# Kernel tuning notes

Measured on AMD Instinct MI355X. Metric: run time of the kernel, lower is better.

The kernel has to match this reference:

```python
import jax, jax.numpy as jnp
import numpy as np
from jax import lax

P = 8       # patch_size
TEMP = 30.0 # softmax temperature from RelationUnit.temp


def _conv3x3(x, w, b, groups):
    # x: [B, C, H, W], w: [O, C//groups, 3, 3]
    y = lax.conv_general_dilated(x, w, (1, 1), 'SAME', feature_group_count=groups)
    return y + b[None, :, None, None]


def _unfold(x):
    # nn.Unfold(kernel=P, stride=P): [B,C,H,W] -> [B, C*P*P, n], channel-major then (ki,kj)
    B, C, H, W = x.shape
    x = x.reshape(B, C, H // P, P, W // P, P)
    x = x.transpose(0, 1, 3, 5, 2, 4)          # [B,C,P,P,H/P,W/P]
    return x.reshape(B, C * P * P, (H // P) * (W // P))


def _fold(x, H, W):
    # inverse of _unfold (non-overlapping patches)
    B, CPP, n = x.shape
    C = CPP // (P * P)
    x = x.reshape(B, C, P, P, H // P, W // P)
    x = x.transpose(0, 1, 4, 2, 5, 3)          # [B,C,H/P,P,W/P,P]
    return x.reshape(B, C, H, W)


def _head(query, key, value, wq, bq, wk, bk, wv, bv):
    # one RelationUnit (heads=1 internally)
    b, tq, c, h, w = query.shape
    t = key.shape[1]
    n = (h // P) * (w // P)
    d = P * P * c

    q = _conv3x3(query.reshape(-1, c, h, w), wq, bq, groups=c)   # depthwise
    k = _conv3x3(key.reshape(-1, c, h, w), wk, bk, groups=c)     # depthwise
    v = _conv3x3(value.reshape(-1, c, h, w), wv, bv, groups=1)   # dense

    # [b*t, d, n] -> [b, d, t*n]  (matches view/permute chain in torch code)
    uq = _unfold(q).reshape(b, tq, d, n).transpose(0, 2, 1, 3).reshape(b, d, tq * n)
    uk = _unfold(k).reshape(b, t, d, n).transpose(0, 2, 1, 3).reshape(b, d, t * n)
    uv = _unfold(v).reshape(b, t, d, n).transpose(0, 2, 1, 3).reshape(b, d, t * n)

    attn = jnp.einsum('bdq,bdk->bqk', uq, uk) * (d ** -0.5)
    attn = jax.nn.softmax(attn * TEMP, axis=-1)
    out = jnp.einsum('bqk,bdk->bqd', attn, uv)                   # [b, tq*n, d]

    out = out.reshape(b, tq, n, d).transpose(0, 1, 3, 2).reshape(b * tq, d, n)
    feat = _fold(out, h, w)                                      # [b*tq, c, h, w]
    return feat.reshape(query.shape)


def reference(query, key, value, Wq, bq, Wk, bk, Wv, bv):
    heads = jax.vmap(_head, in_axes=(None, None, None, 0, 0, 0, 0, 0, 0))(
        query, key, value, Wq, bq, Wk, bk, Wv, bv)               # [Nh, b, tq, c, h, w]
    Nh = heads.shape[0]
    return jnp.concatenate([heads[i] for i in range(Nh)], axis=-1)


def setup_inputs() -> dict:
    key = jax.random.key(0)
    ks = jax.random.split(key, 6)
    b, tq, t, c, h, w, Nh = 1, 2, 2, 32, 224, 336, 4
    f32 = jnp.float32
    rn = lambda k, s, sc=1.0: jax.random.normal(k, s, f32) * sc
    return {
        'query': rn(ks[0], (b, tq, c, h, w)),
        'key':   rn(ks[1], (b, t, c, h, w)),
        'value': rn(ks[2], (b, t, c, h, w)),
        'Wq': rn(ks[3], (Nh, c, 1, 3, 3), 0.1), 'bq': jnp.zeros((Nh, c), f32),
        'Wk': rn(ks[4], (Nh, c, 1, 3, 3), 0.1), 'bk': jnp.zeros((Nh, c), f32),
        'Wv': rn(ks[5], (Nh, c, c, 3, 3), 0.05), 'bv': jnp.zeros((Nh, c), f32),
    }
```

## Files before the change

### kernel.cpp

```cpp
#include <hip/hip_runtime.h>
#include <hip/hip_bf16.h>

#define T_FR 2
#define C_CH 32
#define H_IMG 224
#define W_IMG 336
#define NH 4
#define NPATCH 1176
#define NQ 2352
#define NPAD 2432
#define DD 2048
#define WOUT (W_IMG*NH)
#define SM_SCALE 0.6629126073623885f
#define PIX_F (H_IMG*W_IMG)
#define PIX_T (T_FR*PIX_F)

typedef __attribute__((ext_vector_type(4))) float f32x4;
typedef __attribute__((ext_vector_type(8))) short short8;
typedef unsigned short ushort_t;
typedef __attribute__((ext_vector_type(4))) unsigned short u16x4;
typedef __attribute__((ext_vector_type(8))) unsigned short u16x8;

__device__ inline ushort_t f2bf(float x){
  union { float f; unsigned int u; } v; v.f = x;
  unsigned int r = v.u + 0x7fffu + ((v.u >> 16) & 1u);
  return (ushort_t)(r >> 16);
}

__device__ inline void gload16(const void* g, void* l){
  __builtin_amdgcn_global_load_lds(
      (const __attribute__((address_space(1))) void*)g,
      (__attribute__((address_space(3))) void*)l,
      16, 0, 0);
}

__global__ __launch_bounds__(256) void zero_pads(
    ushort_t* __restrict__ Qu, ushort_t* __restrict__ Ku,
    ushort_t* __restrict__ Vu, int nh)
{
  const int per = 80*DD;
  int tot = 3*nh*per;
  for (int id = blockIdx.x*256 + threadIdx.x; id < tot; id += gridDim.x*256){
    int buf = id / (nh*per);
    int rem = id - buf*(nh*per);
    int h = rem / per;
    int e = rem - h*per;
    ushort_t* B = (buf==0) ? Qu : (buf==1) ? Ku : Vu;
    B[((size_t)h*NPAD + NQ)*DD + e] = 0;
  }
}

__global__ __launch_bounds__(256) void transpose_cl(
    const float* __restrict__ in, ushort_t* __restrict__ inCL)
{
  int id = blockIdx.x*256 + threadIdx.x;
  int t = id / PIX_F;
  int p = id - t*PIX_F;
  const float* src = in + (size_t)t*C_CH*PIX_F + p;
  #pragma unroll
  for (int oct=0; oct<4; oct++){
    u16x8 u;
    #pragma unroll
    for (int e=0; e<8; e++)
      u[e] = f2bf(src[(size_t)(oct*8+e)*PIX_F]);
    *(u16x8*)&inCL[(size_t)id*C_CH + oct*8] = u;
  }
}

__global__ __launch_bounds__(256) void prep_wb(
    const float* __restrict__ Wv, ushort_t* __restrict__ Wb)
{
  int idx = blockIdx.x*256 + threadIdx.x;
  if (idx >= 9*128*32) return;
  int tap = idx >> 12;
  int og  = (idx >> 5) & 127;
  int cc  = idx & 31;
  Wb[idx] = f2bf(Wv[(size_t)og*288 + cc*9 + tap]);
}

__global__ __launch_bounds__(256) void dwconv_unfold(
    const float* __restrict__ in, const float* __restrict__ Wd,
    const float* __restrict__ bd, ushort_t* __restrict__ outU,
    int head0, int nh)
{
  int id = blockIdx.x*256 + threadIdx.x;
  int cc = id & 31;
  int rest = id >> 5;
  int xseg = rest % 42;
  rest /= 42;
  int y = rest % H_IMG;
  int t = rest / H_IMG;

  const float* src = in + ((size_t)(t*C_CH + cc)*H_IMG)*W_IMG;
  int x0 = xseg*8;

  float r0[10], r1[10], r2[10];
  #pragma unroll
  for (int j=0;j<10;j++){
    int xx = x0 + j - 1;
    bool xok = (xx>=0) && (xx<W_IMG);
    r0[j] = (xok && y>0)         ? src[(size_t)(y-1)*W_IMG+xx] : 0.f;
    r1[j] = (xok)                ? src[(size_t)y*W_IMG+xx]     : 0.f;
    r2[j] = (xok && y<H_IMG-1)   ? src[(size_t)(y+1)*W_IMG+xx] : 0.f;
  }
  int qrow = t*NPATCH + (y>>3)*42 + xseg;
  int dcol = (y&7)*256 + cc*8;

  for (int h = 0; h < nh; ++h){
    const float* w = Wd + ((size_t)(head0+h)*C_CH + cc)*9;
    float w0=w[0],w1=w[1],w2=w[2],w3=w[3],w4=w[4],w5=w[5],w6=w[6],w7=w[7],w8=w[8];
    float bias = bd[(size_t)(head0+h)*C_CH + cc];
    u16x8 res;
    #pragma unroll
    for (int j=0;j<8;j++){
      float a = bias;
      a += r0[j]*w0 + r0[j+1]*w1 + r0[j+2]*w2;
      a += r1[j]*w3 + r1[j+1]*w4 + r1[j+2]*w5;
      a += r2[j]*w6 + r2[j+1]*w7 + r2[j+2]*w8;
      res[j] = f2bf(a);
    }
    *(u16x8*)&outU[((size_t)h*NPAD + qrow)*DD + dcol] = res;
  }
}

#define VA_HALO 0
#define VA_BS   37120
#define V_LDS   73984

__global__ __launch_bounds__(256) void vconv_mfma(
    const ushort_t* __restrict__ inCL, const ushort_t* __restrict__ Wb,
    const float* __restrict__ bvv, ushort_t* __restrict__ Vu, int head0)
{
  __shared__ __align__(16) char lds[V_LDS];
  int xt = blockIdx.x;
  int pr_g = blockIdx.y;
  int z  = blockIdx.z;
  int t  = pr_g / 28, pr = pr_g - t*28;
  int x0 = xt*56, y0 = pr*8;
  int tid = threadIdx.x, lane = tid & 63, wid = tid >> 6;

  for (int i = tid; i < 580; i += 256){
    int ly = i/58, lx = i - (i/58)*58;
    int gy = y0 - 1 + ly, gx = x0 - 1 + lx;
    u16x8 v0={},v1={},v2={},v3={};
    if (gy>=0 && gy<H_IMG && gx>=0 && gx<W_IMG){
      const u16x8* s = (const u16x8*)&inCL[((size_t)t*PIX_F + gy*W_IMG + gx)*C_CH];
      v0=s[0]; v1=s[1]; v2=s[2]; v3=s[3];
    }
    *(u16x8*)&lds[VA_HALO + 0*9280 + i*16] = v0;
    *(u16x8*)&lds[VA_HALO + 1*9280 + i*16] = v1;
    *(u16x8*)&lds[VA_HALO + 2*9280 + i*16] = v2;
    *(u16x8*)&lds[VA_HALO + 3*9280 + i*16] = v3;
  }
  for (int i = tid; i < 576; i += 256){
    int tap = i/64, ol = i - (i/64)*64;
    const u16x8* s = (const u16x8*)&Wb[((size_t)tap*128 + head0*32 + z*64 + ol)*C_CH];
    #pragma unroll
    for (int oct=0; oct<4; oct++)
      *(u16x8*)&lds[VA_BS + tap*4096 + ol*64 + ((oct^(ol&3))<<4)] = s[oct];
  }
  __syncthreads();

  int aoff[7];
  #pragma unroll
  for (int m=0;m<7;m++){
    int pm = wid*112 + m*16 + (lane&15);
    int yl = pm/56, xl = pm - yl*56;
    aoff[m] = VA_HALO + (lane>>4)*9280 + (yl*58 + xl)*16;
  }

  f32x4 acc[7][4] = {};
  #pragma unroll
  for (int tap=0; tap<9; tap++){
    const int dy = tap/3, dx = tap - (tap/3)*3;
    short8 bfr[4];
    #pragma unroll
    for (int n=0;n<4;n++){
      int ol = n*16 + (lane&15);
      bfr[n] = *(const short8*)&lds[VA_BS + tap*4096 + ol*64 + ((((lane>>4))^(ol&3))<<4)];
    }
    #pragma unroll
    for (int m=0;m<7;m++){
      short8 af = *(const short8*)&lds[aoff[m] + (dy*58+dx)*16];
      #pragma unroll
      for (int n=0;n<4;n++)
        acc[m][n] = __builtin_amdgcn_mfma_f32_16x16x32_bf16(af, bfr[n], acc[m][n], 0,0,0);
    }
  }
  __syncthreads();

  float bias[4];
  #pragma unroll
  for (int n=0;n<4;n++){
    int ol = n*16 + (lane&15);
    bias[n] = bvv[(size_t)(head0 + z*2 + (ol>>5))*C_CH + (ol&31)];
  }
  #pragma unroll
  for (int m=0;m<7;m++){
    #pragma unroll
    for (int j=0;j<4;j++){
      int p = wid*112 + m*16 + (lane>>4)*4 + j;
      int yl = p/56, xl = p - (p/56)*56;
      int kl = xl >> 3;
      int off = yl*8 + (xl&7);
      #pragma unroll
      for (int n=0;n<4;n++){
        int ol = n*16 + (lane&15);
        int addr = ((ol>>5)*7 + kl)*4096 + (off*32 + (ol&31))*2;
        *(ushort_t*)&lds[addr] = f2bf(acc[m][n][j] + bias[n]);
      }
    }
  }
  __syncthreads();
  int key0 = t*NPATCH + pr*42 + xt*7;
  #pragma unroll
  for (int i=0;i<14;i++){
    int c = i*256 + tid;
    int hib = c / 1792;
    int rem = c - hib*1792;
    int kl = rem >> 8, dch = rem & 255;
    u16x8 v = *(const u16x8*)&lds[c*16];
    *(u16x8*)&Vu[((size_t)(z*2+hib)*NPAD + key0 + kl)*DD + dch*8] = v;
  }
}

__global__ __launch_bounds__(256) void vtranspose(
    const ushort_t* __restrict__ Vu, ushort_t* __restrict__ Vt)
{
  __shared__ ushort_t tile[64*68];
  int d0 = blockIdx.x*64;
  int k0 = blockIdx.y*64;
  const ushort_t* src = Vu + (size_t)blockIdx.z*NPAD*DD;
  ushort_t* dst = Vt + (size_t)blockIdx.z*DD*NPAD;
  int t = threadIdx.x;
  #pragma unroll
  for (int i=0;i<2;i++){
    int key = (t>>3) + i*32;
    int dd  = (t&7)*8;
    u16x8 v = *(const u16x8*)&src[(size_t)(k0+key)*DD + d0+dd];
    #pragma unroll
    for (int e=0;e<8;e++) tile[(dd+e)*68 + key] = v[e];
  }
  __syncthreads();
  #pragma unroll
  for (int i=0;i<2;i++){
    int dd  = (t>>3) + i*32;
    int key = (t&7)*8;
    u16x4 a = *(const u16x4*)&tile[dd*68 + key];
    u16x4 b = *(const u16x4*)&tile[dd*68 + key + 4];
    u16x8 v;
    v[0]=a[0]; v[1]=a[1]; v[2]=a[2]; v[3]=a[3];
    v[4]=b[0]; v[5]=b[1]; v[6]=b[2]; v[7]=b[3];
    *(u16x8*)&dst[(size_t)(d0+dd)*NPAD + k0+key] = v;
  }
}

#define ABASE(b,kc) ((b)*32768 + (kc)*16384)
#define BBASE(b,kc) (65536 + (b)*32768 + (kc)*16384)

#define STG(dstb, Mat, t0, Rm1, ktc) { \
  int i0_ = tid;       int r0_ = i0_>>2; int c0_ = ((i0_&3) ^ ((r0_>>1)&3)); \
  gload16(Mat + (size_t)min(t0 + r0_, Rm1)*(size_t)K + (ktc) + c0_*8, \
          lds + (dstb) + (tid & ~63)*16); \
  int i1_ = 512 + tid; int r1_ = i1_>>2; int c1_ = ((i1_&3) ^ ((r1_>>1)&3)); \
  gload16(Mat + (size_t)min(t0 + r1_, Rm1)*(size_t)K + (ktc) + c1_*8, \
          lds + (dstb) + (512 + (tid & ~63))*16); }

#define RD_A(dst, b, kc, mh) { _Pragma("unroll") \
  for (int m=0;m<4;m++) \
    dst[m] = *(const short8*)(lds + ABASE(b,kc) + (wr*128 + (mh)*64 + m*16 + l15)*64 + rkB); }

#define RD_B(dst, b, kc) { _Pragma("unroll") \
  for (int n=0;n<4;n++) \
    dst[n] = *(const short8*)(lds + BBASE(b,kc) + (wc*64 + n*16 + l15)*64 + rkB); }

#define MFMA32() { __builtin_amdgcn_s_setprio(1); \
  _Pragma("unroll") for (int m=0;m<4;m++){ \
    _Pragma("unroll") for (int n=0;n<4;n++) \
      acc[m][n] = __builtin_amdgcn_mfma_f32_16x16x32_bf16(af[m], bf[n], acc[m][n], 0,0,0); } \
  _Pragma("unroll") for (int m=0;m<4;m++){ \
    _Pragma("unroll") for (int n=0;n<4;n++) \
      acc[4+m][n] = __builtin_amdgcn_mfma_f32_16x16x32_bf16(ag[m], bf[n], acc[4+m][n], 0,0,0); } \
  __builtin_amdgcn_s_setprio(0); }

#define LEADBAR() { __builtin_amdgcn_sched_barrier(0); \
  __builtin_amdgcn_s_barrier(); __builtin_amdgcn_sched_barrier(0); }

#define TRAILBAR() { __builtin_amdgcn_sched_barrier(0); \
  __builtin_amdgcn_s_barrier(); __builtin_amdgcn_sched_barrier(0); }

#define GATEBAR(cond) { __builtin_amdgcn_sched_barrier(0); \
  if (cond) { asm volatile("s_waitcnt vmcnt(4)" ::: "memory"); } \
  else      { asm volatile("s_waitcnt vmcnt(0)" ::: "memory"); } \
  __builtin_amdgcn_s_barrier(); __builtin_amdgcn_sched_barrier(0); }

template<int MODE>
__global__ __launch_bounds__(512) void gemm8p(
    const ushort_t* __restrict__ A, const ushort_t* __restrict__ B,
    float* __restrict__ C, float* __restrict__ Out,
    int K, int Am1, int Bm1, size_t aStr, size_t bStr, int head0)
{
  __shared__ __align__(16) char lds[131072];
  int tid = threadIdx.x, lane = tid & 63, wid = tid >> 6;

  int gx = gridDim.x, gy = gridDim.y;
  int nwg = gx*gy*gridDim.z;
  int id  = (blockIdx.z*gy + blockIdx.y)*gx + blockIdx.x;
  int swz = (id & 7)*(nwg >> 3) + (id >> 3);
  int bx = swz % gx; int tmp = swz / gx;
  int by = tmp % gy; int bz = tmp / gy;

  const ushort_t* Ab = A + (size_t)bz*aStr;
  const ushort_t* Bb = B + (size_t)bz*bStr;
  int row0 = by*256, col0 = bx*256;
  int wr = wid >> 2, wc = wid & 3;
  int l15 = lane & 15;
  int rkB = (((lane>>4) ^ ((l15>>1)&3)) * 16);

  f32x4 acc[8][4] = {};
  int NT = K >> 6;
  int NI = NT >> 1;

  STG(ABASE(0,0), Ab, row0, Am1, 0)
  STG(BBASE(0,0), Bb, col0, Bm1, 0)
  STG(ABASE(0,1), Ab, row0, Am1, 32)
  STG(BBASE(0,1), Bb, col0, Bm1, 32)
  STG(ABASE(1,0), Ab, row0, Am1, 64)
  STG(BBASE(1,0), Bb, col0, Bm1, 64)
  __builtin_amdgcn_sched_barrier(0);
  asm volatile("s_waitcnt vmcnt(4)" ::: "memory");
  __builtin_amdgcn_s_barrier();
  __builtin_amdgcn_sched_barrier(0);

  #pragma unroll 1
  for (int it = 0; it < NI; ++it){
    int T1k = (2*it+1) << 6;
    int T2k = (2*it+2) << 6;
    int T3k = (2*it+3) << 6;
    bool s2 = (2*it+2 < NT), s3 = (2*it+3 < NT);
    short8 af[4], ag[4], bf[4];

    RD_A(af, 0,0,0) RD_A(ag, 0,0,1) RD_B(bf, 0,0)
    STG(ABASE(1,1), Ab, row0, Am1, T1k+32)
    STG(BBASE(1,1), Bb, col0, Bm1, T1k+32)
    LEADBAR() MFMA32() TRAILBAR()
    RD_A(af, 0,1,0) RD_A(ag, 0,1,1) RD_B(bf, 0,1)
    if (s2){ STG(ABASE(0,0), Ab, row0, Am1, T2k)
             STG(BBASE(0,0), Bb, col0, Bm1, T2k) }
    LEADBAR() MFMA32()
    GATEBAR(s2)
    RD_A(af, 1,0,0) RD_A(ag, 1,0,1) RD_B(bf, 1,0)
    if (s2){ STG(ABASE(0,1), Ab, row0, Am1, T2k+32)
             STG(BBASE(0,1), Bb, col0, Bm1, T2k+32) }
    LEADBAR() MFMA32() TRAILBAR()
    RD_A(af, 1,1,0) RD_A(ag, 1,1,1) RD_B(bf, 1,1)
    if (s3){ STG(ABASE(1,0), Ab, row0, Am1, T3k)
             STG(BBASE(1,0), Bb, col0, Bm1, T3k) }
    LEADBAR() MFMA32()
    GATEBAR(s3)
  }
  __builtin_amdgcn_sched_barrier(0);
  asm volatile("s_waitcnt vmcnt(0) lgkmcnt(0)" ::: "memory");
  __builtin_amdgcn_sched_barrier(0);

  int rb0 = row0 + wr*128 + (lane>>4)*4;
  int cb0 = col0 + wc*64 + l15;
  if (MODE == 0){
    float* Cb = C + (size_t)bz*NPAD*(size_t)NPAD;
    #pragma unroll
    for (int M=0;M<8;M++)
      #pragma unroll
      for (int n=0;n<4;n++){
        int col = cb0 + n*16;
        if (col < NPAD)
          #pragma unroll
          for (int j=0;j<4;j++){
            int row = rb0 + M*16 + j;
            if (row < NPAD)
              Cb[(size_t)row*NPAD + col] = acc[M][n][j];
          }
      }
  } else {
    int head = head0 + bz;
    #pragma unroll
    for (int M=0;M<8;M++){
      #pragma unroll
      for (int j=0;j<4;j++){
        int q = rb0 + M*16 + j;
        if (q < NQ){
          int t = q / NPATCH;
          int p = q - t*NPATCH;
          int hi = p / 42, wi = p - hi*42;
          #pragma unroll
          for (int n=0;n<4;n++){
            int dd = cb0 + n*16;
            int cch = dd & 31;
            int off = dd >> 5;
            int pi = off >> 3, pj = off & 7;
            int yy = hi*8 + pi, xx = wi*8 + pj;
            Out[(((size_t)t*C_CH + cch)*H_IMG + yy)*WOUT + (size_t)head*W_IMG + xx]
              = acc[M][n][j];
          }
        }
      }
    }
  }
}

__global__ __launch_bounds__(256) void softmax_rows(
    const float* __restrict__ S, ushort_t* __restrict__ Pm)
{
  const float* row = S + ((size_t)blockIdx.y*NPAD + blockIdx.x)*NPAD;
  ushort_t* prow = Pm + ((size_t)blockIdx.y*NPAD + blockIdx.x)*NPAD;
  int tid = threadIdx.x;
  __shared__ float red[4];
  const f32x4* row4 = (const f32x4*)row;

  bool h2 = (512 + tid) < 588;
  f32x4 v0 = row4[tid];
  f32x4 v1 = row4[256 + tid];
  f32x4 v2 = {-3.0e38f, -3.0e38f, -3.0e38f, -3.0e38f};
  if (h2) v2 = row4[512 + tid];

  float mx = -3.0e38f;
  #pragma unroll
  for (int e=0;e<4;e++) mx = fmaxf(mx, fmaxf(v0[e], fmaxf(v1[e], v2[e])));
  #pragma unroll
  for (int o=32;o;o>>=1) mx = fmaxf(mx, __shfl_xor(mx, o));
  if ((tid&63)==0) red[tid>>6] = mx;
  __syncthreads();
  mx = fmaxf(fmaxf(red[0],red[1]), fmaxf(red[2],red[3]));
  __syncthreads();

  f32x4 e0, e1, e2 = {0.f,0.f,0.f,0.f};
  float s = 0.f;
  #pragma unroll
  for (int e=0;e<4;e++){ e0[e] = __expf((v0[e]-mx)*SM_SCALE); s += e0[e]; }
  #pragma unroll
  for (int e=0;e<4;e++){ e1[e] = __expf((v1[e]-mx)*SM_SCALE); s += e1[e]; }
  if (h2){
    #pragma unroll
    for (int e=0;e<4;e++){ e2[e] = __expf((v2[e]-mx)*SM_SCALE); s += e2[e]; }
  }
  #pragma unroll
  for (int o=32;o;o>>=1) s += __shfl_xor(s, o);
  if ((tid&63)==0) red[tid>>6] = s;
  __syncthreads();
  s = (red[0]+red[1]) + (red[2]+red[3]);
  float inv = 1.0f / s;

  u16x4 o0, o1;
  #pragma unroll
  for (int e=0;e<4;e++) o0[e] = f2bf(e0[e]*inv);
  #pragma unroll
  for (int e=0;e<4;e++) o1[e] = f2bf(e1[e]*inv);
  *(u16x4*)&prow[tid*4]        = o0;
  *(u16x4*)&prow[1024 + tid*4] = o1;
  if (h2){
    u16x4 o2;
    #pragma unroll
    for (int e=0;e<4;e++) o2[e] = f2bf(e2[e]*inv);
    *(u16x4*)&prow[2048 + tid*4] = o2;
  } else if (512 + tid < 608){
    u16x4 z = {0,0,0,0};
    *(u16x4*)&prow[2048 + tid*4] = z;
  }
}

extern "C" void kernel_launch(void* const* d_in, const int* in_sizes, int n_in,
                              void* d_out, int out_size, void* d_ws, size_t ws_size,
                              hipStream_t stream)
{
  const float* query = (const float*)d_in[0];
  const float* key_  = (const float*)d_in[1];
  const float* value = (const float*)d_in[2];
  const float* Wq = (const float*)d_in[3];
  const float* bq = (const float*)d_in[4];
  const float* Wk = (const float*)d_in[5];
  const float* bk = (const float*)d_in[6];
  const float* Wv = (const float*)d_in[7];
  const float* bv = (const float*)d_in[8];
  float* out = (float*)d_out;

  const size_t szU = (size_t)NPAD*DD;
  const size_t szS = (size_t)NPAD*NPAD;
  const size_t perHeadB = 3*szU*sizeof(ushort_t) + szS*sizeof(float) + szS*sizeof(ushort_t);

  int nh = (ws_size >= 4*perHeadB) ? 4 : 2;

  for (int h0 = 0; h0 < NH; h0 += nh){
    char* p = (char*)d_ws;
    ushort_t* Qu = (ushort_t*)p; p += nh*szU*sizeof(ushort_t);
    ushort_t* Ku = (ushort_t*)p; p += nh*szU*sizeof(ushort_t);
    ushort_t* Vu = (ushort_t*)p; p += nh*szU*sizeof(ushort_t);
    float*    S  = (float*)p;    p += nh*szS*sizeof(float);
    ushort_t* Pm = (ushort_t*)p;
    ushort_t* inCL = (ushort_t*)S;
    ushort_t* Wb   = inCL + (size_t)PIX_T*C_CH;
    ushort_t* Vt   = Qu;

    zero_pads<<<dim3(960), dim3(256), 0, stream>>>(Qu, Ku, Vu, nh);
    transpose_cl<<<dim3(588), dim3(256), 0, stream>>>(value, inCL);
    prep_wb<<<dim3(144), dim3(256), 0, stream>>>(Wv, Wb);
    dwconv_unfold<<<dim3(2352), dim3(256), 0, stream>>>(query, Wq, bq, Qu, h0, nh);
    dwconv_unfold<<<dim3(2352), dim3(256), 0, stream>>>(key_,  Wk, bk, Ku, h0, nh);
    vconv_mfma<<<dim3(6, 56, nh/2), dim3(256), 0, stream>>>(inCL, Wb, bv, Vu, h0);
    gemm8p<0><<<dim3(10, 10, nh), dim3(512), 0, stream>>>(
        Qu, Ku, S, nullptr, DD, NPAD-1, NPAD-1, szU, szU, h0);
    vtranspose<<<dim3(32, 38, nh), dim3(256), 0, stream>>>(Vu, Vt);
    softmax_rows<<<dim3(NPAD, nh), dim3(256), 0, stream>>>(S, Pm);
    gemm8p<1><<<dim3(8, 10, nh), dim3(512), 0, stream>>>(
        Pm, Vt, nullptr, out, NPAD, NPAD-1, DD-1, szS, szU, h0);
  }
}
```

Measured before the change: 496.2 us.

## Replace deep LDS pipeline with simple double-buffered 32-wide K loop in GEMM

Rewrites the main GEMM loop to stage one 32-wide K slice per step into a two-slot LDS buffer. This replaces the previous four-stage 64-wide schedule with partial vmcnt waits and halves LDS use from 128 KB to 64 KB, which may allow more resident workgroups per CU. In exchange each step now waits for all outstanding loads (vmcnt(0)) and has more barriers per unit of MFMA work, so less global-load latency is hidden.

```diff
diff --git a/kernel.cpp b/kernel.cpp
--- a/kernel.cpp
+++ b/kernel.cpp
@@ -255,8 +255,8 @@
   }
 }
 
-#define ABASE(b,kc) ((b)*32768 + (kc)*16384)
-#define BBASE(b,kc) (65536 + (b)*32768 + (kc)*16384)
+#define ABASE2(b) ((b)*16384)
+#define BBASE2(b) (32768 + (b)*16384)
 
 #define STG(dstb, Mat, t0, Rm1, ktc) { \
   int i0_ = tid;       int r0_ = i0_>>2; int c0_ = ((i0_&3) ^ ((r0_>>1)&3)); \
@@ -266,32 +266,25 @@
   gload16(Mat + (size_t)min(t0 + r1_, Rm1)*(size_t)K + (ktc) + c1_*8, \
           lds + (dstb) + (512 + (tid & ~63))*16); }
 
-#define RD_A(dst, b, kc, mh) { _Pragma("unroll") \
+#define RD_A(dst, b, mh) { _Pragma("unroll") \
   for (int m=0;m<4;m++) \
-    dst[m] = *(const short8*)(lds + ABASE(b,kc) + (wr*128 + (mh)*64 + m*16 + l15)*64 + rkB); }
-
-#define RD_B(dst, b, kc) { _Pragma("unroll") \
+    dst[m] = *(const short8*)(lds + ABASE2(b) + (wr*128 + (mh)*64 + m*16 + l15)*64 + rkB); }
+
+#define RD_B(dst, b) { _Pragma("unroll") \
   for (int n=0;n<4;n++) \
-    dst[n] = *(const short8*)(lds + BBASE(b,kc) + (wc*64 + n*16 + l15)*64 + rkB); }
-
-#define MFMA32() { __builtin_amdgcn_s_setprio(1); \
+    dst[n] = *(const short8*)(lds + BBASE2(b) + (wc*64 + n*16 + l15)*64 + rkB); }
+
+#define DO_MFMA(afS, bfS, mh) { __builtin_amdgcn_s_setprio(1); \
   _Pragma("unroll") for (int m=0;m<4;m++){ \
     _Pragma("unroll") for (int n=0;n<4;n++) \
-      acc[m][n] = __builtin_amdgcn_mfma_f32_16x16x32_bf16(af[m], bf[n], acc[m][n], 0,0,0); } \
-  _Pragma("unroll") for (int m=0;m<4;m++){ \
-    _Pragma("unroll") for (int n=0;n<4;n++) \
-      acc[4+m][n] = __builtin_amdgcn_mfma_f32_16x16x32_bf16(ag[m], bf[n], acc[4+m][n], 0,0,0); } \
+      acc[(mh)*4+m][n] = __builtin_amdgcn_mfma_f32_16x16x32_bf16(afS[m], bfS[n], acc[(mh)*4+m][n], 0,0,0); } \
   __builtin_amdgcn_s_setprio(0); }
 
-#define LEADBAR() { __builtin_amdgcn_sched_barrier(0); \
+#define BAR() { __builtin_amdgcn_sched_barrier(0); \
   __builtin_amdgcn_s_barrier(); __builtin_amdgcn_sched_barrier(0); }
 
-#define TRAILBAR() { __builtin_amdgcn_sched_barrier(0); \
-  __builtin_amdgcn_s_barrier(); __builtin_amdgcn_sched_barrier(0); }
-
-#define GATEBAR(cond) { __builtin_amdgcn_sched_barrier(0); \
-  if (cond) { asm volatile("s_waitcnt vmcnt(4)" ::: "memory"); } \
-  else      { asm volatile("s_waitcnt vmcnt(0)" ::: "memory"); } \
+#define GATE0() { __builtin_amdgcn_sched_barrier(0); \
+  asm volatile("s_waitcnt vmcnt(0)" ::: "memory"); \
   __builtin_amdgcn_s_barrier(); __builtin_amdgcn_sched_barrier(0); }
 
 template<int MODE>
@@ -300,7 +293,7 @@
     float* __restrict__ C, float* __restrict__ Out,
     int K, int Am1, int Bm1, size_t aStr, size_t bStr, int head0)
 {
-  __shared__ __align__(16) char lds[131072];
+  __shared__ __align__(16) char lds[65536];
   int tid = threadIdx.x, lane = tid & 63, wid = tid >> 6;
 
   int gx = gridDim.x, gy = gridDim.y;
@@ -318,46 +311,34 @@
   int rkB = (((lane>>4) ^ ((l15>>1)&3)) * 16);
 
   f32x4 acc[8][4] = {};
-  int NT = K >> 6;
-  int NI = NT >> 1;
-
-  STG(ABASE(0,0), Ab, row0, Am1, 0)
-  STG(BBASE(0,0), Bb, col0, Bm1, 0)
-  STG(ABASE(0,1), Ab, row0, Am1, 32)
-  STG(BBASE(0,1), Bb, col0, Bm1, 32)
-  STG(ABASE(1,0), Ab, row0, Am1, 64)
-  STG(BBASE(1,0), Bb, col0, Bm1, 64)
+  int NT = K >> 5;
+
+  STG(ABASE2(0), Ab, row0, Am1, 0)
+  STG(BBASE2(0), Bb, col0, Bm1, 0)
   __builtin_amdgcn_sched_barrier(0);
-  asm volatile("s_waitcnt vmcnt(4)" ::: "memory");
+  asm volatile("s_waitcnt vmcnt(0)" ::: "memory");
   __builtin_amdgcn_s_barrier();
   __builtin_amdgcn_sched_barrier(0);
 
   #pragma unroll 1
-  for (int it = 0; it < NI; ++it){
-    int T1k = (2*it+1) << 6;
-    int T2k = (2*it+2) << 6;
-    int T3k = (2*it+3) << 6;
-    bool s2 = (2*it+2 < NT), s3 = (2*it+3 < NT);
+  for (int t = 0; t < NT; ++t){
+    int b = t & 1, nb = b ^ 1;
+    bool more = (t + 1 < NT);
     short8 af[4], ag[4], bf[4];
 
-    RD_A(af, 0,0,0) RD_A(ag, 0,0,1) RD_B(bf, 0,0)
-    STG(ABASE(1,1), Ab, row0, Am1, T1k+32)
-    STG(BBASE(1,1), Bb, col0, Bm1, T1k+32)
-    LEADBAR() MFMA32() TRAILBAR()
-    RD_A(af, 0,1,0) RD_A(ag, 0,1,1) RD_B(bf, 0,1)
-    if (s2){ STG(ABASE(0,0), Ab, row0, Am1, T2k)
-             STG(BBASE(0,0), Bb, col0, Bm1, T2k) }
-    LEADBAR() MFMA32()
-    GATEBAR(s2)
-    RD_A(af, 1,0,0) RD_A(ag, 1,0,1) RD_B(bf, 1,0)
-    if (s2){ STG(ABASE(0,1), Ab, row0, Am1, T2k+32)
-             STG(BBASE(0,1), Bb, col0, Bm1, T2k+32) }
-    LEADBAR() MFMA32() TRAILBAR()
-    RD_A(af, 1,1,0) RD_A(ag, 1,1,1) RD_B(bf, 1,1)
-    if (s3){ STG(ABASE(1,0), Ab, row0, Am1, T3k)
-             STG(BBASE(1,0), Bb, col0, Bm1, T3k) }
-    LEADBAR() MFMA32()
-    GATEBAR(s3)
+    RD_A(af, b, 0) RD_B(bf, b)
+    if (more){
+      int ktn = (t+1) << 5;
+      STG(ABASE2(nb), Ab, row0, Am1, ktn)
+      STG(BBASE2(nb), Bb, col0, Bm1, ktn)
+    }
+    BAR()
+    DO_MFMA(af, bf, 0)
+    BAR()
+    RD_A(ag, b, 1)
+    BAR()
+    DO_MFMA(ag, bf, 1)
+    GATE0()
   }
   __builtin_amdgcn_sched_barrier(0);
   asm volatile("s_waitcnt vmcnt(0) lgkmcnt(0)" ::: "memory");
```

Result: slower. 512.6 us (+3.3%).
